# Performance work log

Hardware: AMD Instinct MI355X
Metric: run time of the kernel (lower is better)

The kernel has to match this reference:

```python
import jax, jax.numpy as jnp
import numpy as np

IN_FEATURES = 4096
OUT_FEATURES = 4096
BLOCK_SIZE = 64
BLOCK_NUM = 64
N_FACTORS = 3  # boft_n_butterfly_factor


def _butterfly_perm(n, b, r):
    # Mirrors BOFTLayer.block_butterfly_perm for n_butterfly_factor != 0.
    block_size = n // b
    step = block_size // r
    evens = np.arange(0, step, 2)
    odds = np.arange(1, step, 2)
    seq = np.concatenate([evens, odds])
    sorted_order = np.concatenate([np.arange(p * r, p * r + r) for p in seq])
    return np.arange(n).reshape(-1, block_size)[:, sorted_order].reshape(-1)


def setup_inputs() -> dict:
    key = jax.random.key(0)
    k1, k2, k3, k4, k5 = jax.random.split(key, 5)
    x = jax.random.normal(k1, (8, 2048, IN_FEATURES), dtype=jnp.float32)
    weight = jax.random.normal(k2, (OUT_FEATURES, IN_FEATURES), dtype=jnp.float32) * 0.02
    bias = jax.random.normal(k3, (OUT_FEATURES,), dtype=jnp.float32) * 0.02
    boft_R = jax.random.normal(k4, (N_FACTORS, BLOCK_NUM, BLOCK_SIZE, BLOCK_SIZE), dtype=jnp.float32) * 0.1
    boft_s = jax.random.uniform(k5, (OUT_FEATURES, 1), dtype=jnp.float32, minval=0.5, maxval=1.5)
    perm = jnp.asarray(np.stack([
        _butterfly_perm(IN_FEATURES, BLOCK_NUM // (2 ** i), BLOCK_SIZE // 2)
        for i in range(N_FACTORS)
    ]), dtype=jnp.int32)
    return {"x": x, "weight": weight, "bias": bias, "boft_R": boft_R,
            "boft_s": boft_s, "perm": perm}


def _cayley(R):
    # Q = (I - skew) @ inv(I + skew), skew = (R - R^T)/2; batched.
    skew = 0.5 * (R - jnp.swapaxes(R, -1, -2))
    I = jnp.eye(R.shape[-1], dtype=R.dtype)
    # Right-division via solve: X (I+skew) = (I-skew)
    Xt = jnp.linalg.solve(jnp.swapaxes(I + skew, -1, -2), jnp.swapaxes(I - skew, -1, -2))
    return jnp.swapaxes(Xt, -1, -2)


def _block_diag(blocks):
    # (D, H, H) -> (D*H, D*H) block-diagonal
    D, H, _ = blocks.shape
    out = jnp.zeros((D, H, D, H), blocks.dtype)
    out = out.at[jnp.arange(D), :, jnp.arange(D), :].set(blocks)
    return out.reshape(D * H, D * H)


def reference(x, weight, bias, boft_R, boft_s, perm):
    N, D, H, _ = boft_R.shape
    Q = _cayley(boft_R.reshape(N * D, H, H)).reshape(N, D, H, H)
    # P_i @ block_diag_i @ P_i^T implemented as a symmetric gather (P is a permutation)
    rot = None
    for i in range(N):  # small fixed loop over butterfly factors
        bd = _block_diag(Q[i])
        p = perm[i]
        mat = bd[p][:, p]  # (in, in)
        rot = mat if rot is None else mat @ rot
    # rotated_weight = (rot @ W^T)^T = W @ rot^T ; then scale rows by boft_s
    scaled_w = (weight @ rot.T) * boft_s  # (out, in)
    return x @ scaled_w.T + bias
```

## Files before the change

kernel.cpp:

```cpp
#include <hip/hip_runtime.h>
#include <hip/hip_bf16.h>
#include <cstddef>
#include <cstdint>

#define IN_F 4096
#define OUT_F 4096

typedef __attribute__((ext_vector_type(8))) _Float16 half8;
typedef __attribute__((ext_vector_type(4))) float f32x4;

__global__ __launch_bounds__(256) void cayley_kernel(const float* __restrict__ R,
                                                     float* __restrict__ Qs) {
  __shared__ float Mm[64][65];
  __shared__ float Bm[64][65];
  const int b = blockIdx.x;
  const float* Rb = R + (size_t)b * 4096;
  const int t = threadIdx.x;
  const int i = t >> 2;
  const int jb = (t & 3) << 4;

  #pragma unroll 4
  for (int q = 0; q < 16; ++q) {
    int j = jb + q;
    float rij = Rb[i * 64 + j];
    float rji = Rb[j * 64 + i];
    float sk = 0.5f * (rij - rji);
    float id = (i == j) ? 1.0f : 0.0f;
    Mm[i][j] = id - sk;
    Bm[i][j] = id + sk;
  }
  __syncthreads();

  for (int k = 0; k < 64; ++k) {
    float inv = 1.0f / Mm[k][k];
    float f = Mm[i][k];
    __syncthreads();
    if (t < 64) {
      Mm[k][t] *= inv;
      Bm[k][t] *= inv;
    }
    __syncthreads();
    if (i != k) {
      #pragma unroll 4
      for (int q = 0; q < 16; ++q) {
        int j = jb + q;
        Mm[i][j] = fmaf(-f, Mm[k][j], Mm[i][j]);
        Bm[i][j] = fmaf(-f, Bm[k][j], Bm[i][j]);
      }
    }
    __syncthreads();
  }

  float* out = Qs + (size_t)b * 4096;
  #pragma unroll 4
  for (int q = 0; q < 16; ++q) {
    int flat = t * 16 + q;
    out[flat] = Bm[flat >> 6][flat & 63];
  }
}

__global__ void invperm_kernel(const int* __restrict__ perm,
                               int* __restrict__ ip1, int* __restrict__ ip2) {
  int c = blockIdx.x * 256 + threadIdx.x;
  ip1[perm[4096 + c]] = c;
  ip2[perm[8192 + c]] = c;
}

__global__ void compose_kernel(const int* __restrict__ perm,
                               const int* __restrict__ ip1,
                               const int* __restrict__ ip2,
                               int* __restrict__ rho1, int* __restrict__ rho2) {
  int k = blockIdx.x * 256 + threadIdx.x;
  rho1[k] = perm[ip1[k]];
  rho2[k] = perm[4096 + ip2[k]];
}

__global__ __launch_bounds__(256) void transpose_perm_kernel(const float* __restrict__ W,
                                                             const int* __restrict__ p0,
                                                             float* __restrict__ U0) {
  __shared__ float tile[64][65];
  const int c0 = blockIdx.x * 64;
  const int n0 = blockIdx.y * 64;
  const int t = threadIdx.x;
  const int r = t >> 2;
  const int cb = (t & 3) << 4;
  #pragma unroll
  for (int q = 0; q < 4; ++q) {
    float4 v = *(const float4*)(W + (size_t)(n0 + r) * IN_F + c0 + cb + q * 4);
    tile[r][cb + q * 4 + 0] = v.x;
    tile[r][cb + q * 4 + 1] = v.y;
    tile[r][cb + q * 4 + 2] = v.z;
    tile[r][cb + q * 4 + 3] = v.w;
  }
  __syncthreads();
  const int c = t >> 2;
  const int nb = (t & 3) << 4;
  const int dstrow = p0[c0 + c];
  #pragma unroll
  for (int q = 0; q < 4; ++q) {
    float4 v;
    v.x = tile[nb + q * 4 + 0][c];
    v.y = tile[nb + q * 4 + 1][c];
    v.z = tile[nb + q * 4 + 2][c];
    v.w = tile[nb + q * 4 + 3][c];
    *(float4*)(U0 + (size_t)dstrow * OUT_F + n0 + nb + q * 4) = v;
  }
}

__global__ __launch_bounds__(256) void factor_kernel(const float* __restrict__ src,
                                                     float* __restrict__ dst,
                                                     const float* __restrict__ Qt,
                                                     const int* __restrict__ rowIdx,
                                                     const int* __restrict__ dstIdx,
                                                     const float* __restrict__ s) {
  __shared__ float qt[64][64];
  __shared__ int sidx[64];
  __shared__ int didx[64];
  const int g = blockIdx.y;
  const int n0 = blockIdx.x * 256;
  const int t = threadIdx.x;

  {
    const float* qg = Qt + (size_t)g * 4096;
    float4* qv = (float4*)&qt[0][0];
    #pragma unroll
    for (int q = 0; q < 4; ++q)
      qv[t * 4 + q] = *(const float4*)(qg + t * 16 + q * 4);
  }
  if (t < 64) {
    sidx[t] = rowIdx ? rowIdx[g * 64 + t] : g * 64 + t;
    didx[t] = dstIdx ? dstIdx[g * 64 + t] : g * 64 + t;
  }
  __syncthreads();

  const int w = t >> 6;
  const int lane = t & 63;
  const int nOff = n0 + lane * 4;
  float4 a[16];
  #pragma unroll
  for (int ii = 0; ii < 16; ++ii) a[ii] = make_float4(0.f, 0.f, 0.f, 0.f);

  for (int j = 0; j < 64; ++j) {
    float4 v = *(const float4*)(src + (size_t)sidx[j] * OUT_F + nOff);
    const float* qr = &qt[j][w * 16];
    #pragma unroll
    for (int ii = 0; ii < 16; ++ii) {
      float qq = qr[ii];
      a[ii].x = fmaf(qq, v.x, a[ii].x);
      a[ii].y = fmaf(qq, v.y, a[ii].y);
      a[ii].z = fmaf(qq, v.z, a[ii].z);
      a[ii].w = fmaf(qq, v.w, a[ii].w);
    }
  }

  float4 sv = make_float4(1.f, 1.f, 1.f, 1.f);
  if (s) sv = *(const float4*)(s + nOff);
  #pragma unroll
  for (int ii = 0; ii < 16; ++ii) {
    int r = didx[w * 16 + ii];
    float4 o;
    o.x = a[ii].x * sv.x; o.y = a[ii].y * sv.y;
    o.z = a[ii].z * sv.z; o.w = a[ii].w * sv.w;
    *(float4*)(dst + (size_t)r * OUT_F + nOff) = o;
  }
}

__global__ __launch_bounds__(256) void transpose_cvt_kernel(const float* __restrict__ S,
                                                            _Float16* __restrict__ D) {
  __shared__ float tile[64][65];
  const int k0 = blockIdx.x * 64;
  const int n0 = blockIdx.y * 64;
  const int t = threadIdx.x;
  const int r = t >> 2;
  const int cb = (t & 3) << 4;
  #pragma unroll
  for (int q = 0; q < 4; ++q) {
    float4 v = *(const float4*)(S + (size_t)(k0 + r) * OUT_F + n0 + cb + q * 4);
    tile[r][cb + q * 4 + 0] = v.x;
    tile[r][cb + q * 4 + 1] = v.y;
    tile[r][cb + q * 4 + 2] = v.z;
    tile[r][cb + q * 4 + 3] = v.w;
  }
  __syncthreads();
  const int n = t >> 2;
  const int kb = (t & 3) << 4;
  half8 h0, h1;
  #pragma unroll
  for (int q = 0; q < 8; ++q) {
    h0[q] = (_Float16)tile[kb + q][n];
    h1[q] = (_Float16)tile[kb + 8 + q][n];
  }
  _Float16* dp = D + (size_t)(n0 + n) * IN_F + k0 + kb;
  *(half8*)dp = h0;
  *(half8*)(dp + 8) = h1;
}

#define GBM 128
#define GBN 128
#define GBK 32

__global__ __launch_bounds__(256) void mfma_gemm(const float* __restrict__ A,
                                                 const _Float16* __restrict__ Bh,
                                                 const float* __restrict__ bias,
                                                 float* __restrict__ C, int M) {
  __shared__ _Float16 Ash[GBM * GBK];
  __shared__ _Float16 Bsh[GBN * GBK];
  const int t = threadIdx.x;
  const int lane = t & 63;
  const int w = t >> 6;
  const int wr = w >> 1;
  const int wc = w & 1;
  const int m0 = blockIdx.y * GBM;
  const int n0 = blockIdx.x * GBN;
  const int K = IN_F;
  const int N = OUT_F;

  f32x4 acc[4][4];
  #pragma unroll
  for (int i = 0; i < 4; ++i)
    #pragma unroll
    for (int j = 0; j < 4; ++j) acc[i][j] = (f32x4){0.f, 0.f, 0.f, 0.f};

  const int srow = t >> 2;
  const int skc = (t & 3) << 3;

  const int frow = lane & 15;
  const int fk = (lane >> 4) << 3;

  for (int k0 = 0; k0 < K; k0 += GBK) {
    #pragma unroll
    for (int p = 0; p < 2; ++p) {
      const _Float16* gb = Bh + (size_t)(n0 + srow + p * 64) * K + k0 + skc;
      _Float16* lb = Bsh + ((size_t)(t & ~63) + p * 256) * 8;
      __builtin_amdgcn_global_load_lds(
          (const __attribute__((address_space(1))) uint32_t*)gb,
          (__attribute__((address_space(3))) uint32_t*)lb, 16, 0, 0);
    }
    #pragma unroll
    for (int p = 0; p < 2; ++p) {
      const float* ga = A + (size_t)(m0 + srow + p * 64) * K + k0 + skc;
      f32x4 v0 = *(const f32x4*)ga;
      f32x4 v1 = *(const f32x4*)(ga + 4);
      half8 h;
      h[0] = (_Float16)v0.x; h[1] = (_Float16)v0.y;
      h[2] = (_Float16)v0.z; h[3] = (_Float16)v0.w;
      h[4] = (_Float16)v1.x; h[5] = (_Float16)v1.y;
      h[6] = (_Float16)v1.z; h[7] = (_Float16)v1.w;
      *(half8*)(Ash + ((size_t)t + p * 256) * 8) = h;
    }
    __syncthreads();

    half8 af[4], bf[4];
    #pragma unroll
    for (int i = 0; i < 4; ++i)
      af[i] = *(const half8*)(Ash + (wr * 64 + i * 16 + frow) * GBK + fk);
    #pragma unroll
    for (int j = 0; j < 4; ++j)
      bf[j] = *(const half8*)(Bsh + (wc * 64 + j * 16 + frow) * GBK + fk);
    #pragma unroll
    for (int i = 0; i < 4; ++i)
      #pragma unroll
      for (int j = 0; j < 4; ++j)
        acc[i][j] = __builtin_amdgcn_mfma_f32_16x16x32_f16(af[i], bf[j], acc[i][j], 0, 0, 0);
    __syncthreads();
  }

  const int crow = (lane >> 4) << 2;
  const int ccol = lane & 15;
  #pragma unroll
  for (int j = 0; j < 4; ++j) {
    int n = n0 + wc * 64 + j * 16 + ccol;
    float bv = bias[n];
    #pragma unroll
    for (int i = 0; i < 4; ++i) {
      int mbase = m0 + wr * 64 + i * 16 + crow;
      #pragma unroll
      for (int r = 0; r < 4; ++r)
        C[(size_t)(mbase + r) * N + n] = acc[i][j][r] + bv;
    }
  }
}

extern "C" void kernel_launch(void* const* d_in, const int* in_sizes, int n_in,
                              void* d_out, int out_size, void* d_ws, size_t ws_size,
                              hipStream_t stream) {
  const float* x      = (const float*)d_in[0];
  const float* weight = (const float*)d_in[1];
  const float* bias   = (const float*)d_in[2];
  const float* boft_R = (const float*)d_in[3];
  const float* boft_s = (const float*)d_in[4];
  const int*   perm   = (const int*)d_in[5];
  float* out = (float*)d_out;

  float* ws   = (float*)d_ws;
  float* Qs   = ws;
  float* bufA = ws + 786432;
  float* bufB = bufA + 16777216;
  int*   ints = (int*)(bufB + 16777216);
  int* ip1  = ints;
  int* ip2  = ints + 4096;
  int* rho1 = ints + 8192;
  int* rho2 = ints + 12288;

  const int M = in_sizes[0] / IN_F;

  hipLaunchKernelGGL(cayley_kernel, dim3(192), dim3(256), 0, stream, boft_R, Qs);
  hipLaunchKernelGGL(invperm_kernel, dim3(16), dim3(256), 0, stream, perm, ip1, ip2);
  hipLaunchKernelGGL(compose_kernel, dim3(16), dim3(256), 0, stream, perm, ip1, ip2, rho1, rho2);
  hipLaunchKernelGGL(transpose_perm_kernel, dim3(64, 64), dim3(256), 0, stream,
                     weight, perm, bufA);
  hipLaunchKernelGGL(factor_kernel, dim3(16, 64), dim3(256), 0, stream,
                     bufA, bufB, Qs, (const int*)nullptr, (const int*)nullptr,
                     (const float*)nullptr);
  hipLaunchKernelGGL(factor_kernel, dim3(16, 64), dim3(256), 0, stream,
                     bufB, bufA, Qs + 262144, rho1, (const int*)nullptr,
                     (const float*)nullptr);
  hipLaunchKernelGGL(factor_kernel, dim3(16, 64), dim3(256), 0, stream,
                     bufA, bufB, Qs + 524288, rho2, ip2, boft_s);
  _Float16* Bh = (_Float16*)bufA;
  hipLaunchKernelGGL(transpose_cvt_kernel, dim3(64, 64), dim3(256), 0, stream,
                     bufB, Bh);
  hipLaunchKernelGGL(mfma_gemm, dim3(OUT_F / GBN, M / GBM), dim3(256), 0, stream,
                     x, Bh, bias, out, M);
}
```

Before: 1.450 ms.

## Rewrite main GEMM with 256x256 tiles, 4-stage async LDS pipeline and pre-converted fp16 x

Converts x to fp16 in a separate pass and stores both fp16 operands with an XOR swizzle on 16-byte chunks, so the GEMM can load both A and B straight into LDS with global_load_lds. The new GEMM uses 256x256 tiles with 8 waves, a 4-slot LDS ring with explicit vmcnt waits and barriers, s_setprio around the MFMA block, and a grouped block-index remap for L2 locality. The aim is to hide global memory latency, raise arithmetic intensity, and avoid the in-loop fp32 to fp16 conversion and LDS bank conflicts. The cost is an extra pass over x to write a 128 MB fp16 copy, higher register and LDS pressure, and a hard-coded loop count that assumes K=4096.

```diff
diff --git a/kernel.cpp b/kernel.cpp
--- a/kernel.cpp
+++ b/kernel.cpp
@@ -165,8 +165,8 @@
   }
 }
 
-__global__ __launch_bounds__(256) void transpose_cvt_kernel(const float* __restrict__ S,
-                                                            _Float16* __restrict__ D) {
+__global__ __launch_bounds__(256) void transpose_cvt_swz(const float* __restrict__ S,
+                                                         _Float16* __restrict__ D) {
   __shared__ float tile[64][65];
   const int k0 = blockIdx.x * 64;
   const int n0 = blockIdx.y * 64;
@@ -190,80 +190,135 @@
     h0[q] = (_Float16)tile[kb + q][n];
     h1[q] = (_Float16)tile[kb + 8 + q][n];
   }
-  _Float16* dp = D + (size_t)(n0 + n) * IN_F + k0 + kb;
-  *(half8*)dp = h0;
-  *(half8*)(dp + 8) = h1;
-}
-
-#define GBM 128
-#define GBN 128
-#define GBK 32
-
-__global__ __launch_bounds__(256) void mfma_gemm(const float* __restrict__ A,
-                                                 const _Float16* __restrict__ Bh,
-                                                 const float* __restrict__ bias,
-                                                 float* __restrict__ C, int M) {
-  __shared__ _Float16 Ash[GBM * GBK];
-  __shared__ _Float16 Bsh[GBN * GBK];
+  const int gn = n0 + n;
+  const int sw = gn & 3;
+  const int c0 = (k0 + kb) >> 3;
+  const int c0s = (c0 & ~3) | ((c0 & 3) ^ sw);
+  const int c1s = (c0 & ~3) | (((c0 + 1) & 3) ^ sw);
+  _Float16* dp = D + (size_t)gn * IN_F;
+  *(half8*)(dp + c0s * 8) = h0;
+  *(half8*)(dp + c1s * 8) = h1;
+}
+
+__global__ __launch_bounds__(256) void cvt_x_kernel(const float* __restrict__ X,
+                                                    _Float16* __restrict__ Ah) {
+  const int idx = blockIdx.x * 256 + threadIdx.x;
+  const int m = idx >> 9;
+  const int c = idx & 511;
+  const float* xp = X + (size_t)m * IN_F + c * 8;
+  f32x4 v0 = *(const f32x4*)xp;
+  f32x4 v1 = *(const f32x4*)(xp + 4);
+  half8 h;
+  h[0] = (_Float16)v0.x; h[1] = (_Float16)v0.y;
+  h[2] = (_Float16)v0.z; h[3] = (_Float16)v0.w;
+  h[4] = (_Float16)v1.x; h[5] = (_Float16)v1.y;
+  h[6] = (_Float16)v1.z; h[7] = (_Float16)v1.w;
+  const int cs = (c & ~3) | ((c & 3) ^ (m & 3));
+  *(half8*)(Ah + (size_t)m * IN_F + cs * 8) = h;
+}
+
+#define TM 256
+#define TN 256
+#define TK 32
+#define NSLOT 4
+
+typedef const __attribute__((address_space(1))) uint32_t* gptr_t;
+typedef __attribute__((address_space(3))) uint32_t* lptr_t;
+
+#define WB(n) asm volatile("s_waitcnt vmcnt(" #n ")\ns_barrier" ::: "memory")
+
+__global__ __launch_bounds__(512, 2) void mfma_gemm2(const _Float16* __restrict__ A,
+                                                     const _Float16* __restrict__ B,
+                                                     const float* __restrict__ bias,
+                                                     float* __restrict__ C, int M) {
+  __shared__ __align__(16) _Float16 lds[NSLOT][2][TM * TK];
   const int t = threadIdx.x;
   const int lane = t & 63;
   const int w = t >> 6;
-  const int wr = w >> 1;
-  const int wc = w & 1;
-  const int m0 = blockIdx.y * GBM;
-  const int n0 = blockIdx.x * GBN;
-  const int K = IN_F;
-  const int N = OUT_F;
-
-  f32x4 acc[4][4];
-  #pragma unroll
-  for (int i = 0; i < 4; ++i)
+  const int wr = w >> 2;
+  const int wc = w & 3;
+
+  const int nwg = gridDim.x * gridDim.y;
+  const int lin = blockIdx.y * gridDim.x + blockIdx.x;
+  const int cpx = nwg >> 3;
+  const int nl = (lin & 7) * cpx + (lin >> 3);
+  const int n0 = (nl & 15) * TN;
+  const int m0 = (nl >> 4) * TM;
+
+  const _Float16* gA[2];
+  const _Float16* gB[2];
+  int ldsoff[2];
+  #pragma unroll
+  for (int p = 0; p < 2; ++p) {
+    int chunk = p * 512 + t;
+    int row = chunk >> 2;
+    int c = chunk & 3;
+    gA[p] = A + (size_t)(m0 + row) * IN_F + c * 8;
+    gB[p] = B + (size_t)(n0 + row) * IN_F + c * 8;
+    ldsoff[p] = (p * 512 + (t & ~63)) * 8;
+  }
+
+  const int frow = lane & 15;
+  const int kc = lane >> 4;
+  int aoff[8], boff[4];
+  #pragma unroll
+  for (int i = 0; i < 8; ++i) {
+    int r = wr * 128 + i * 16 + frow;
+    aoff[i] = r * TK + ((kc ^ (r & 3)) << 3);
+  }
+  #pragma unroll
+  for (int j = 0; j < 4; ++j) {
+    int r = wc * 64 + j * 16 + frow;
+    boff[j] = r * TK + ((kc ^ (r & 3)) << 3);
+  }
+
+  f32x4 acc[8][4];
+  #pragma unroll
+  for (int i = 0; i < 8; ++i)
     #pragma unroll
     for (int j = 0; j < 4; ++j) acc[i][j] = (f32x4){0.f, 0.f, 0.f, 0.f};
 
-  const int srow = t >> 2;
-  const int skc = (t & 3) << 3;
-
-  const int frow = lane & 15;
-  const int fk = (lane >> 4) << 3;
-
-  for (int k0 = 0; k0 < K; k0 += GBK) {
-    #pragma unroll
-    for (int p = 0; p < 2; ++p) {
-      const _Float16* gb = Bh + (size_t)(n0 + srow + p * 64) * K + k0 + skc;
-      _Float16* lb = Bsh + ((size_t)(t & ~63) + p * 256) * 8;
-      __builtin_amdgcn_global_load_lds(
-          (const __attribute__((address_space(1))) uint32_t*)gb,
-          (__attribute__((address_space(3))) uint32_t*)lb, 16, 0, 0);
-    }
-    #pragma unroll
-    for (int p = 0; p < 2; ++p) {
-      const float* ga = A + (size_t)(m0 + srow + p * 64) * K + k0 + skc;
-      f32x4 v0 = *(const f32x4*)ga;
-      f32x4 v1 = *(const f32x4*)(ga + 4);
-      half8 h;
-      h[0] = (_Float16)v0.x; h[1] = (_Float16)v0.y;
-      h[2] = (_Float16)v0.z; h[3] = (_Float16)v0.w;
-      h[4] = (_Float16)v1.x; h[5] = (_Float16)v1.y;
-      h[6] = (_Float16)v1.z; h[7] = (_Float16)v1.w;
-      *(half8*)(Ash + ((size_t)t + p * 256) * 8) = h;
-    }
-    __syncthreads();
-
-    half8 af[4], bf[4];
-    #pragma unroll
-    for (int i = 0; i < 4; ++i)
-      af[i] = *(const half8*)(Ash + (wr * 64 + i * 16 + frow) * GBK + fk);
-    #pragma unroll
-    for (int j = 0; j < 4; ++j)
-      bf[j] = *(const half8*)(Bsh + (wc * 64 + j * 16 + frow) * GBK + fk);
-    #pragma unroll
-    for (int i = 0; i < 4; ++i)
-      #pragma unroll
-      for (int j = 0; j < 4; ++j)
-        acc[i][j] = __builtin_amdgcn_mfma_f32_16x16x32_f16(af[i], bf[j], acc[i][j], 0, 0, 0);
-    __syncthreads();
-  }
+#define STAGE(tt, ss)                                                          \
+  do {                                                                         \
+    _Float16* sA = &lds[ss][0][0];                                             \
+    _Float16* sB = &lds[ss][1][0];                                             \
+    _Pragma("unroll") for (int p = 0; p < 2; ++p) {                            \
+      __builtin_amdgcn_global_load_lds((gptr_t)(gA[p] + (tt) * TK),            \
+                                       (lptr_t)(sA + ldsoff[p]), 16, 0, 0);    \
+      __builtin_amdgcn_global_load_lds((gptr_t)(gB[p] + (tt) * TK),            \
+                                       (lptr_t)(sB + ldsoff[p]), 16, 0, 0);    \
+    }                                                                          \
+  } while (0)
+
+#define COMPUTE(ss)                                                            \
+  do {                                                                         \
+    const _Float16* As = &lds[ss][0][0];                                       \
+    const _Float16* Bs = &lds[ss][1][0];                                       \
+    half8 af[8], bf[4];                                                        \
+    _Pragma("unroll") for (int i = 0; i < 8; ++i)                              \
+        af[i] = *(const half8*)(As + aoff[i]);                                 \
+    _Pragma("unroll") for (int j = 0; j < 4; ++j)                              \
+        bf[j] = *(const half8*)(Bs + boff[j]);                                 \
+    __builtin_amdgcn_s_setprio(1);                                             \
+    _Pragma("unroll") for (int i = 0; i < 8; ++i)                              \
+      _Pragma("unroll") for (int j = 0; j < 4; ++j)                            \
+          acc[i][j] = __builtin_amdgcn_mfma_f32_16x16x32_f16(af[i], bf[j],     \
+                                                             acc[i][j], 0, 0, 0); \
+    __builtin_amdgcn_s_setprio(0);                                             \
+  } while (0)
+
+  STAGE(0, 0);
+  STAGE(1, 1);
+  STAGE(2, 2);
+  WB(8);
+  for (int tt = 0; tt < 125; ++tt) {
+    STAGE(tt + 3, (tt + 3) & 3);
+    COMPUTE(tt & 3);
+    WB(8);
+  }
+  COMPUTE(1); WB(4);
+  COMPUTE(2); WB(0);
+  COMPUTE(3);
 
   const int crow = (lane >> 4) << 2;
   const int ccol = lane & 15;
@@ -272,13 +327,15 @@
     int n = n0 + wc * 64 + j * 16 + ccol;
     float bv = bias[n];
     #pragma unroll
-    for (int i = 0; i < 4; ++i) {
-      int mbase = m0 + wr * 64 + i * 16 + crow;
+    for (int i = 0; i < 8; ++i) {
+      int mbase = m0 + wr * 128 + i * 16 + crow;
       #pragma unroll
       for (int r = 0; r < 4; ++r)
-        C[(size_t)(mbase + r) * N + n] = acc[i][j][r] + bv;
+        C[(size_t)(mbase + r) * OUT_F + n] = acc[i][j][r] + bv;
     }
   }
+#undef STAGE
+#undef COMPUTE
 }
 
 extern "C" void kernel_launch(void* const* d_in, const int* in_sizes, int n_in,
@@ -296,11 +353,13 @@
   float* Qs   = ws;
   float* bufA = ws + 786432;
   float* bufB = bufA + 16777216;
-  int*   ints = (int*)(bufB + 16777216);
+  _Float16* Bh = (_Float16*)(bufB + 16777216);
+  int*   ints = (int*)(Bh + 16777216);
   int* ip1  = ints;
   int* ip2  = ints + 4096;
   int* rho1 = ints + 8192;
   int* rho2 = ints + 12288;
+  _Float16* Ah = (_Float16*)bufA;
 
   const int M = in_sizes[0] / IN_F;
 
@@ -317,9 +376,10 @@
                      (const float*)nullptr);
   hipLaunchKernelGGL(factor_kernel, dim3(16, 64), dim3(256), 0, stream,
                      bufA, bufB, Qs + 524288, rho2, ip2, boft_s);
-  _Float16* Bh = (_Float16*)bufA;
-  hipLaunchKernelGGL(transpose_cvt_kernel, dim3(64, 64), dim3(256), 0, stream,
+  hipLaunchKernelGGL(transpose_cvt_swz, dim3(64, 64), dim3(256), 0, stream,
                      bufB, Bh);
-  hipLaunchKernelGGL(mfma_gemm, dim3(OUT_F / GBN, M / GBM), dim3(256), 0, stream,
-                     x, Bh, bias, out, M);
-}
+  hipLaunchKernelGGL(cvt_x_kernel, dim3((M * IN_F / 8) / 256), dim3(256), 0, stream,
+                     x, Ah);
+  hipLaunchKernelGGL(mfma_gemm2, dim3(OUT_F / TN, M / TM), dim3(512), 0, stream,
+                     Ah, Bh, bias, out, M);
+}
```

Result: faster. 1.195 ms (-17.6%).
